# Performance work log

Hardware: AMD Instinct MI355X
Metric: run time of the kernel (lower is better)

The kernel has to match this reference:

```python
import math
import jax, jax.numpy as jnp
import numpy as np

N, C_S, C_Z, C, H, PQK, PV = 768, 384, 128, 16, 12, 4, 8
INF, EPS = 100000.0, 1e-8


def _quat_to_rot(q):
    # q: [N,4] normalized quaternions -> [N,3,3] rotation matrices
    w, x, y, z = q[:, 0], q[:, 1], q[:, 2], q[:, 3]
    return jnp.stack([
        jnp.stack([1 - 2 * (y * y + z * z), 2 * (x * y - w * z), 2 * (x * z + w * y)], -1),
        jnp.stack([2 * (x * y + w * z), 1 - 2 * (x * x + z * z), 2 * (y * z - w * x)], -1),
        jnp.stack([2 * (x * z - w * y), 2 * (y * z + w * x), 1 - 2 * (x * x + y * y)], -1),
    ], -2)


def setup_inputs() -> dict:
    key = jax.random.key(0)
    ks = jax.random.split(key, 16)
    quat = jax.random.normal(ks[2], (N, 4))
    quat = quat / jnp.linalg.norm(quat, axis=-1, keepdims=True)
    sc = 0.02
    return {
        "s": jax.random.normal(ks[0], (N, C_S), jnp.float32),
        "z": jax.random.normal(ks[1], (N, N, C_Z), jnp.float32),
        "rot": _quat_to_rot(quat).astype(jnp.float32),
        "trans": jax.random.normal(ks[3], (N, 3), jnp.float32),
        "mask": jnp.ones((N,), jnp.float32),
        "Wq": sc * jax.random.normal(ks[4], (C_S, H * C), jnp.float32),
        "bq": jnp.zeros((H * C,), jnp.float32),
        "Wqp": sc * jax.random.normal(ks[5], (C_S, H * 3 * PQK), jnp.float32),
        "bqp": jnp.zeros((H * 3 * PQK,), jnp.float32),
        "Wkv": sc * jax.random.normal(ks[6], (C_S, 2 * H * C), jnp.float32),
        "bkv": jnp.zeros((2 * H * C,), jnp.float32),
        "Wkvp": sc * jax.random.normal(ks[7], (C_S, H * 3 * (PQK + PV)), jnp.float32),
        "bkvp": jnp.zeros((H * 3 * (PQK + PV),), jnp.float32),
        "Wb": sc * jax.random.normal(ks[8], (C_Z, H), jnp.float32),
        "bb": jnp.zeros((H,), jnp.float32),
        "head_weights": 0.5413 * jnp.ones((H,), jnp.float32),  # softplus^{-1}(1)
        "Wout": sc * jax.random.normal(ks[9], (H * (C_Z + C + PV * 4), C_S), jnp.float32),
        "bout": jnp.zeros((C_S,), jnp.float32),
    }


def _proj_points(x, W, b, rot, trans, P):
    # PointProjection: split last dim into 3 coord chunks, stack as last axis
    pl = x @ W + b                                   # [N, H*3*P]
    pl = pl.reshape(-1, 3, H * P).transpose(0, 2, 1).reshape(-1, H, P, 3)
    return jnp.einsum('nij,nhpj->nhpi', rot, pl) + trans[:, None, None, :]


def reference(s, z, rot, trans, mask, Wq, bq, Wqp, bqp, Wkv, bkv, Wkvp, bkvp,
              Wb, bb, head_weights, Wout, bout):
    q = (s @ Wq + bq).reshape(N, H, C)
    kv = (s @ Wkv + bkv).reshape(N, H, 2 * C)
    k, v = kv[..., :C], kv[..., C:]
    q_pts = _proj_points(s, Wqp, bqp, rot, trans, PQK)          # [N,H,PQK,3]
    kv_pts = _proj_points(s, Wkvp, bkvp, rot, trans, PQK + PV)  # [N,H,PQK+PV,3]
    k_pts, v_pts = kv_pts[..., :PQK, :], kv_pts[..., PQK:, :]

    b_bias = z @ Wb + bb                                        # [N,N,H]
    a = jnp.einsum('qhc,khc->hqk', q, k) * math.sqrt(1.0 / (3 * C))
    a = a + math.sqrt(1.0 / 3) * jnp.transpose(b_bias, (2, 0, 1))

    # point-distance attention: [q,k,H,PQK]
    d2 = jnp.sum((q_pts[:, None] - k_pts[None]) ** 2, axis=-1)
    hw = jax.nn.softplus(head_weights) * math.sqrt(1.0 / (3 * (PQK * 9.0 / 2)))
    pt_att = -0.5 * jnp.sum(d2 * hw[:, None], axis=-1)          # [q,k,H]
    a = a + jnp.transpose(pt_att, (2, 0, 1))

    sq_mask = INF * (mask[:, None] * mask[None, :] - 1.0)       # [q,k]
    a = jax.nn.softmax(a + sq_mask[None], axis=-1)              # [H,q,k]

    o = jnp.einsum('hqk,khc->qhc', a, v).reshape(N, H * C)
    o_pt = jnp.einsum('hqk,khpd->qhpd', a, v_pts)               # [q,H,PV,3]
    o_pt = jnp.einsum('nji,nhpj->nhpi', rot, o_pt - trans[:, None, None, :])  # invert_apply
    o_pt_norm = jnp.sqrt(jnp.sum(o_pt ** 2, -1) + EPS).reshape(N, H * PV)
    o_pt_flat = o_pt.reshape(N, H * PV, 3)
    o_pair = jnp.einsum('hqk,qkc->qhc', a, z).reshape(N, H * C_Z)

    cat = jnp.concatenate(
        [o, o_pt_flat[..., 0], o_pt_flat[..., 1], o_pt_flat[..., 2], o_pt_norm, o_pair], -1)
    return cat @ Wout + bout
```

## Files before the change

kernel.cpp:

```cpp
#include <hip/hip_runtime.h>
#include <math.h>

#define NN    768
#define CS    384
#define INF_  100000.0f

#define OFF_Q       0
#define OFF_K       147456
#define OFF_V       294912
#define OFF_QPRAW   442368
#define OFF_KVPRAW  552960
#define OFF_QPTS    884736
#define OFF_KPTS    995328
#define OFF_VPTS    1105920
#define OFF_CAT     8414208

__global__ void __launch_bounds__(256)
k1_proj(const float* __restrict__ s,
        const float* __restrict__ Wq,  const float* __restrict__ bq,
        const float* __restrict__ Wqp, const float* __restrict__ bqp,
        const float* __restrict__ Wkv, const float* __restrict__ bkv,
        const float* __restrict__ Wkvp,const float* __restrict__ bkvp,
        float* __restrict__ ws) {
  __shared__ float s_lds[8][CS];
  const int n0 = blockIdx.y * 8;
  const int j0 = blockIdx.x * 32;
  const int t  = threadIdx.x;

  const float4* s4  = (const float4*)(s + (size_t)n0 * CS);
  float4*       sl4 = (float4*)(&s_lds[0][0]);
  for (int i = t; i < 768; i += 256) sl4[i] = s4[i];
  __syncthreads();

  const int m = t >> 5;
  const int j = j0 + (t & 31);

  const float* W; const float* bv; int jj, ncols;
  if (j < 192)      { W = Wq;   bv = bq;   jj = j;       ncols = 192; }
  else if (j < 576) { W = Wkv;  bv = bkv;  jj = j - 192; ncols = 384; }
  else if (j < 720) { W = Wqp;  bv = bqp;  jj = j - 576; ncols = 144; }
  else              { W = Wkvp; bv = bkvp; jj = j - 720; ncols = 432; }

  float acc = bv[jj];
  const float* Wp = W + jj;
  for (int c = 0; c < CS; ++c) acc += s_lds[m][c] * Wp[(size_t)c * ncols];

  const int n = n0 + m;
  if (j < 192) {
    (ws + OFF_Q)[n * 192 + jj] = acc;
  } else if (j < 576) {
    int h = jj >> 5, c = jj & 31;
    if (c < 16) (ws + OFF_K)[n * 192 + h * 16 + c] = acc;
    else        (ws + OFF_V)[n * 192 + h * 16 + (c - 16)] = acc;
  } else if (j < 720) {
    (ws + OFF_QPRAW)[n * 144 + jj] = acc;
  } else {
    (ws + OFF_KVPRAW)[n * 432 + jj] = acc;
  }
}

__global__ void __launch_bounds__(256)
k2_rot(const float* __restrict__ rot, const float* __restrict__ trans,
       float* __restrict__ ws) {
  const int idx = blockIdx.x * 256 + threadIdx.x;
  const int n = idx / 192;
  const int r = idx % 192;
  const float* R = rot + n * 9;
  const float* T = trans + n * 3;
  if (r < 48) {
    const float* raw = ws + OFF_QPRAW + n * 144;
    float p0 = raw[r], p1 = raw[48 + r], p2 = raw[96 + r];
    float g0 = R[0]*p0 + R[1]*p1 + R[2]*p2 + T[0];
    float g1 = R[3]*p0 + R[4]*p1 + R[5]*p2 + T[1];
    float g2 = R[6]*p0 + R[7]*p1 + R[8]*p2 + T[2];
    float* qp = ws + OFF_QPTS + n * 144 + r * 3;
    qp[0] = g0; qp[1] = g1; qp[2] = g2;
  } else {
    const int r2 = r - 48;
    const float* raw = ws + OFF_KVPRAW + n * 432;
    float p0 = raw[r2], p1 = raw[144 + r2], p2 = raw[288 + r2];
    float g0 = R[0]*p0 + R[1]*p1 + R[2]*p2 + T[0];
    float g1 = R[3]*p0 + R[4]*p1 + R[5]*p2 + T[1];
    float g2 = R[6]*p0 + R[7]*p1 + R[8]*p2 + T[2];
    const int h = r2 / 12, p = r2 % 12;
    if (p < 4) {
      float* kp = ws + OFF_KPTS + n * 144 + (h * 4 + p) * 3;
      kp[0] = g0; kp[1] = g1; kp[2] = g2;
    } else {
      float* vp = ws + OFF_VPTS + n * 288 + (h * 8 + (p - 4)) * 3;
      vp[0] = g0; vp[1] = g1; vp[2] = g2;
    }
  }
}

__global__ void __launch_bounds__(256, 4)
k3_fused(const float* __restrict__ z, const float* __restrict__ rot,
         const float* __restrict__ trans, const float* __restrict__ mask,
         const float* __restrict__ Wb, const float* __restrict__ bb,
         const float* __restrict__ hwin, float* __restrict__ ws) {
  const int q = blockIdx.x, t = threadIdx.x;
  const int g  = __builtin_amdgcn_readfirstlane(t >> 6);
  const int kl = t & 63;
  const int kx = kl & 31;

  __shared__ float4 z4[64][32];
  __shared__ float  w_s[64][12];
  __shared__ float  hw_l[12], bb_l[12], lsum[12], linv[12];
  __shared__ float  opt_raw[288];

  if (t < 12) {
    hw_l[t] = logf(1.0f + expf(hwin[t])) * 0.13608276348795434f;
    bb_l[t] = bb[t];
  }

  const float maskq  = mask[q];
  const float* qrow  = ws + OFF_Q    + q * 192;
  const float* qprow = ws + OFF_QPTS + q * 144;
  const float* kbase = ws + OFF_K;
  const float* kpbase= ws + OFF_KPTS;
  const float* vbase = ws + OFF_V;
  const float* vpbase= ws + OFF_VPTS;
  const float4* zg4  = (const float4*)z + (size_t)q * 24576;

  float l3[3] = {0.f, 0.f, 0.f};
  float op[12];
  #pragma unroll
  for (int j = 0; j < 12; ++j) op[j] = 0.f;
  float oa[4] = {0.f, 0.f, 0.f, 0.f};

  const int tt = t - 128;
  int o_c = 0, o_hq = 0, p_r = 0, p_hq = 0;
  if (tt >= 0 && tt < 48)        { o_c = tt & 15; o_hq = tt >> 4; }
  else if (tt >= 48 && tt < 120) { int jt = tt - 48; p_r = jt % 24; p_hq = jt / 24; }

  for (int k0 = 0; k0 < NN; k0 += 64) {
    __syncthreads();

    #pragma unroll
    for (int j = 0; j < 8; ++j) {
      const int i = t + 256 * j;
      const int row = i >> 5, c4 = i & 31;
      z4[row][c4 ^ (row & 31)] = zg4[k0 * 32 + i];
    }
    __syncthreads();

    {
      float b0 = 0.f, b1 = 0.f, b2 = 0.f;
      #pragma unroll 8
      for (int c4 = 0; c4 < 32; ++c4) {
        const float4 zv = z4[kl][c4 ^ kx];
        const float* wb = Wb + c4 * 48;
        b0 += zv.x*wb[g]    + zv.y*wb[12+g]  + zv.z*wb[24+g]  + zv.w*wb[36+g];
        b1 += zv.x*wb[4+g]  + zv.y*wb[16+g]  + zv.z*wb[28+g]  + zv.w*wb[40+g];
        b2 += zv.x*wb[8+g]  + zv.y*wb[20+g]  + zv.z*wb[32+g]  + zv.w*wb[44+g];
      }
      const int kg = k0 + kl;
      const float mterm = INF_ * (maskq * mask[kg] - 1.0f);
      const float* Kr  = kbase  + kg * 192;
      const float* KPr = kpbase + kg * 144;
      const float bias3[3] = {b0, b1, b2};
      #pragma unroll
      for (int j = 0; j < 3; ++j) {
        const int h = g + 4 * j;
        const float4* K4 = (const float4*)(Kr + h * 16);
        float qk = 0.f;
        #pragma unroll
        for (int c4i = 0; c4i < 4; ++c4i) {
          const float4 kv = K4[c4i];
          const float* qp = qrow + h * 16 + c4i * 4;
          qk += kv.x*qp[0] + kv.y*qp[1] + kv.z*qp[2] + kv.w*qp[3];
        }
        const float4* KP4 = (const float4*)(KPr + h * 12);
        float pt = 0.f;
        #pragma unroll
        for (int r = 0; r < 3; ++r) {
          const float4 kp = KP4[r];
          const float* qpp = qprow + h * 12 + r * 4;
          const float d0 = qpp[0]-kp.x, d1 = qpp[1]-kp.y, d2 = qpp[2]-kp.z, d3 = qpp[3]-kp.w;
          pt += d0*d0 + d1*d1 + d2*d2 + d3*d3;
        }
        const float logit = 0.14433756729740643f * qk
                          + 0.57735026918962576f * (bias3[j] + bb_l[h])
                          - 0.5f * hw_l[h] * pt + mterm;
        const float wv = __expf(logit);
        w_s[kl][h] = wv;
        l3[j] += wv;
      }
    }
    __syncthreads();

    if (t < 128) {
      float wreg[12];
      {
        const float4* wrow = (const float4*)&w_s[kl][0];
        const float4 wa = wrow[0], wbb = wrow[1], wc = wrow[2];
        wreg[0]=wa.x;  wreg[1]=wa.y;  wreg[2]=wa.z;  wreg[3]=wa.w;
        wreg[4]=wbb.x; wreg[5]=wbb.y; wreg[6]=wbb.z; wreg[7]=wbb.w;
        wreg[8]=wc.x;  wreg[9]=wc.y;  wreg[10]=wc.z; wreg[11]=wc.w;
      }
      const int cq = t >> 2, ce = t & 3;
      const float* zb = (const float*)z4;
      #pragma unroll 8
      for (int k = 0; k < 64; ++k) {
        const float zv = zb[k * 128 + ((cq ^ (k & 31)) << 2) + ce];
        #pragma unroll
        for (int j = 0; j < 12; ++j) {
          const float wkj = __uint_as_float(
              __builtin_amdgcn_readlane(__float_as_uint(wreg[j]), k));
          op[j] += wkj * zv;
        }
      }
    } else if (tt < 48) {
      const float* Vp = vbase + (o_hq * 4) * 16 + o_c;
      #pragma unroll 4
      for (int k = 0; k < 64; ++k) {
        const float4 wv4 = *(const float4*)&w_s[k][o_hq * 4];
        const float* vr = Vp + (size_t)(k0 + k) * 192;
        oa[0] += wv4.x * vr[0];
        oa[1] += wv4.y * vr[16];
        oa[2] += wv4.z * vr[32];
        oa[3] += wv4.w * vr[48];
      }
    } else if (tt < 120) {
      const float* VPp = vpbase + (p_hq * 4) * 24 + p_r;
      #pragma unroll 4
      for (int k = 0; k < 64; ++k) {
        const float4 wv4 = *(const float4*)&w_s[k][p_hq * 4];
        const float* vr = VPp + (size_t)(k0 + k) * 288;
        oa[0] += wv4.x * vr[0];
        oa[1] += wv4.y * vr[24];
        oa[2] += wv4.z * vr[48];
        oa[3] += wv4.w * vr[72];
      }
    }
  }

  #pragma unroll
  for (int j = 0; j < 3; ++j) {
    float v = l3[j];
    for (int off = 1; off < 64; off <<= 1) v += __shfl_xor(v, off, 64);
    l3[j] = v;
  }
  if ((t & 63) == 0) { lsum[g] = l3[0]; lsum[g + 4] = l3[1]; lsum[g + 8] = l3[2]; }
  __syncthreads();
  if (t < 12) linv[t] = 1.0f / lsum[t];
  __syncthreads();

  float* cat = ws + OFF_CAT + (size_t)q * 2112;
  if (t < 128) {
    #pragma unroll
    for (int j = 0; j < 12; ++j) cat[576 + j * 128 + t] = op[j] * linv[j];
  } else if (tt < 48) {
    #pragma unroll
    for (int e = 0; e < 4; ++e)
      cat[(o_hq * 4 + e) * 16 + o_c] = oa[e] * linv[o_hq * 4 + e];
  } else if (tt < 120) {
    #pragma unroll
    for (int e = 0; e < 4; ++e)
      opt_raw[(p_hq * 4 + e) * 24 + p_r] = oa[e] * linv[p_hq * 4 + e];
  }
  __syncthreads();

  if (t < 96) {
    const int h = t >> 3, p = t & 7;
    const float* R = rot + q * 9;
    const float* T = trans + q * 3;
    const float g0 = opt_raw[h * 24 + p * 3 + 0] - T[0];
    const float g1 = opt_raw[h * 24 + p * 3 + 1] - T[1];
    const float g2 = opt_raw[h * 24 + p * 3 + 2] - T[2];
    const float x  = R[0]*g0 + R[3]*g1 + R[6]*g2;
    const float y  = R[1]*g0 + R[4]*g1 + R[7]*g2;
    const float zc = R[2]*g0 + R[5]*g1 + R[8]*g2;
    const int hp = h * 8 + p;
    cat[192 + hp] = x;
    cat[288 + hp] = y;
    cat[384 + hp] = zc;
    cat[480 + hp] = sqrtf(x*x + y*y + zc*zc + 1e-8f);
  }
}

__global__ void __launch_bounds__(256)
k5_out(const float* __restrict__ Wout, const float* __restrict__ bout,
       const float* __restrict__ ws, float* __restrict__ out) {
  __shared__ float cat_lds[4 * 2112];
  const int m0 = blockIdx.y * 4;
  const int n0 = blockIdx.x * 64;
  const int t  = threadIdx.x;

  const float4* c4  = (const float4*)(ws + OFF_CAT + (size_t)m0 * 2112);
  float4*       cl4 = (float4*)cat_lds;
  for (int i = t; i < 2112; i += 256) cl4[i] = c4[i];
  __syncthreads();

  const int m = t >> 6, nn = n0 + (t & 63);
  const float* cm = cat_lds + m * 2112;
  float acc = bout[nn];
  for (int k = 0; k < 2112; ++k) acc += cm[k] * Wout[(size_t)k * 384 + nn];
  out[(size_t)(m0 + m) * 384 + nn] = acc;
}

extern "C" void kernel_launch(void* const* d_in, const int* in_sizes, int n_in,
                              void* d_out, int out_size, void* d_ws, size_t ws_size,
                              hipStream_t stream) {
  const float* s     = (const float*)d_in[0];
  const float* z     = (const float*)d_in[1];
  const float* rot   = (const float*)d_in[2];
  const float* trans = (const float*)d_in[3];
  const float* mask  = (const float*)d_in[4];
  const float* Wq    = (const float*)d_in[5];
  const float* bq    = (const float*)d_in[6];
  const float* Wqp   = (const float*)d_in[7];
  const float* bqp   = (const float*)d_in[8];
  const float* Wkv   = (const float*)d_in[9];
  const float* bkv   = (const float*)d_in[10];
  const float* Wkvp  = (const float*)d_in[11];
  const float* bkvp  = (const float*)d_in[12];
  const float* Wb    = (const float*)d_in[13];
  const float* bb    = (const float*)d_in[14];
  const float* hw    = (const float*)d_in[15];
  const float* Wout  = (const float*)d_in[16];
  const float* bout  = (const float*)d_in[17];
  float* out = (float*)d_out;
  float* ws  = (float*)d_ws;

  k1_proj<<<dim3(36, 96), 256, 0, stream>>>(s, Wq, bq, Wqp, bqp, Wkv, bkv, Wkvp, bkvp, ws);
  k2_rot <<<576, 256, 0, stream>>>(rot, trans, ws);
  k3_fused<<<NN, 256, 0, stream>>>(z, rot, trans, mask, Wb, bb, hw, ws);
  k5_out<<<dim3(6, 192), 256, 0, stream>>>(Wout, bout, ws, out);
}
```

Before: 797.5 us.

## Use bf16 MFMA for pair bias and pair output, tile output GEMM with split-K

The fused attention kernel now converts each z tile to bf16 in two LDS layouts and uses MFMA 16x16x32 instructions for both the z·Wb pair bias and the weighted sum over z. K and key points are pre-transposed by a new kernel so logits read coalesced columns. The work of accumulating over V and V-points is redistributed across all threads. The output projection becomes a 64x64 register-tiled GEMM with 4-way split-K and atomicAdd onto a bias-initialised output. bf16 rounding of z and of the attention weights lowers precision, and the atomics make the output order-dependent.

```diff
diff --git a/kernel.cpp b/kernel.cpp
--- a/kernel.cpp
+++ b/kernel.cpp
@@ -4,6 +4,9 @@
 #define NN    768
 #define CS    384
 #define INF_  100000.0f
+
+typedef __attribute__((ext_vector_type(8))) short s16x8;
+typedef __attribute__((ext_vector_type(4))) float f32x4;
 
 #define OFF_Q       0
 #define OFF_K       147456
@@ -13,7 +16,17 @@
 #define OFF_QPTS    884736
 #define OFF_KPTS    995328
 #define OFF_VPTS    1105920
+#define OFF_KT      1327104
+#define OFF_KPT     1474560
 #define OFF_CAT     8414208
+
+__device__ __forceinline__ unsigned short f2bf(float x) {
+  unsigned u = __float_as_uint(x) + 0x8000u;
+  return (unsigned short)(u >> 16);
+}
+__device__ __forceinline__ unsigned pk2(float a, float b) {
+  return (unsigned)f2bf(a) | ((unsigned)f2bf(b) << 16);
+}
 
 __global__ void __launch_bounds__(256)
 k1_proj(const float* __restrict__ s,
@@ -93,144 +106,174 @@
   }
 }
 
-__global__ void __launch_bounds__(256, 4)
+__global__ void __launch_bounds__(256)
+k2b_tr(float* __restrict__ ws) {
+  const int i = blockIdx.x * 256 + threadIdx.x;
+  if (i < 147456) {
+    const int n = i / 192, cc = i % 192;
+    (ws + OFF_KT)[cc * 768 + n] = (ws + OFF_K)[i];
+  } else {
+    const int i2 = i - 147456;
+    const int n = i2 / 144, r = i2 % 144;
+    (ws + OFF_KPT)[r * 768 + n] = (ws + OFF_KPTS)[i2];
+  }
+}
+
+#define ZT_S 72
+#define ZR_S 136
+#define WT_S 72
+#define WH_S 68
+__global__ void __launch_bounds__(256, 3)
 k3_fused(const float* __restrict__ z, const float* __restrict__ rot,
          const float* __restrict__ trans, const float* __restrict__ mask,
          const float* __restrict__ Wb, const float* __restrict__ bb,
          const float* __restrict__ hwin, float* __restrict__ ws) {
   const int q = blockIdx.x, t = threadIdx.x;
-  const int g  = __builtin_amdgcn_readfirstlane(t >> 6);
-  const int kl = t & 63;
-  const int kx = kl & 31;
-
-  __shared__ float4 z4[64][32];
-  __shared__ float  w_s[64][12];
-  __shared__ float  hw_l[12], bb_l[12], lsum[12], linv[12];
-  __shared__ float  opt_raw[288];
+  const int g   = t >> 6;
+  const int kl  = t & 63;
+  const int l15 = kl & 15, lq = kl >> 4;
+
+  __shared__ unsigned short zT[128 * ZT_S];
+  __shared__ unsigned short zR[64 * ZR_S];
+  __shared__ unsigned short wT[16 * WT_S];
+  __shared__ float wH[12 * WH_S];
+  __shared__ float bias_s[64 * 13];
+  __shared__ float hw_l[12], bb_l[12], lsum[12], linv[12];
+  __shared__ float opt_raw[288];
 
   if (t < 12) {
     hw_l[t] = logf(1.0f + expf(hwin[t])) * 0.13608276348795434f;
     bb_l[t] = bb[t];
   }
 
+  s16x8 wbA[4];
+  #pragma unroll
+  for (int kk = 0; kk < 4; ++kk) {
+    #pragma unroll
+    for (int j = 0; j < 8; ++j) {
+      float v = (l15 < 12) ? Wb[(kk * 32 + lq * 8 + j) * 12 + l15] : 0.0f;
+      wbA[kk][j] = (short)f2bf(v);
+    }
+  }
+
   const float maskq  = mask[q];
   const float* qrow  = ws + OFF_Q    + q * 192;
   const float* qprow = ws + OFF_QPTS + q * 144;
-  const float* kbase = ws + OFF_K;
-  const float* kpbase= ws + OFF_KPTS;
+  const float* ktr   = ws + OFF_KT;
+  const float* kptr  = ws + OFF_KPT;
   const float* vbase = ws + OFF_V;
   const float* vpbase= ws + OFF_VPTS;
   const float4* zg4  = (const float4*)z + (size_t)q * 24576;
 
   float l3[3] = {0.f, 0.f, 0.f};
-  float op[12];
-  #pragma unroll
-  for (int j = 0; j < 12; ++j) op[j] = 0.f;
-  float oa[4] = {0.f, 0.f, 0.f, 0.f};
-
-  const int tt = t - 128;
-  int o_c = 0, o_hq = 0, p_r = 0, p_hq = 0;
-  if (tt >= 0 && tt < 48)        { o_c = tt & 15; o_hq = tt >> 4; }
-  else if (tt >= 48 && tt < 120) { int jt = tt - 48; p_r = jt % 24; p_hq = jt / 24; }
+  f32x4 opA = {0.f,0.f,0.f,0.f}, opB = {0.f,0.f,0.f,0.f};
+  float o_acc = 0.f;
+  float pt0 = 0.f, pt1 = 0.f;
+  const int oh  = t >> 4;
+  const int ph  = t / 24,        prr = t % 24;
+  const int p2s = 256 + t, p2h = p2s / 24;
 
   for (int k0 = 0; k0 < NN; k0 += 64) {
     __syncthreads();
 
+    float4 zv[8];
+    #pragma unroll
+    for (int j = 0; j < 8; ++j) zv[j] = zg4[k0 * 32 + t + 256 * j];
+    const int kb = t >> 5, c4 = t & 31;
     #pragma unroll
     for (int j = 0; j < 8; ++j) {
-      const int i = t + 256 * j;
-      const int row = i >> 5, c4 = i & 31;
-      z4[row][c4 ^ (row & 31)] = zg4[k0 * 32 + i];
+      uint2 d;
+      d.x = pk2(zv[j].x, zv[j].y);
+      d.y = pk2(zv[j].z, zv[j].w);
+      *(uint2*)&zR[(kb + 8 * j) * ZR_S + c4 * 4] = d;
+    }
+    #pragma unroll
+    for (int e = 0; e < 4; ++e) {
+      uint4 d;
+      d.x = pk2(((const float*)&zv[0])[e], ((const float*)&zv[1])[e]);
+      d.y = pk2(((const float*)&zv[2])[e], ((const float*)&zv[3])[e]);
+      d.z = pk2(((const float*)&zv[4])[e], ((const float*)&zv[5])[e]);
+      d.w = pk2(((const float*)&zv[6])[e], ((const float*)&zv[7])[e]);
+      *(uint4*)&zT[(c4 * 4 + e) * ZT_S + kb * 8] = d;
     }
     __syncthreads();
 
     {
-      float b0 = 0.f, b1 = 0.f, b2 = 0.f;
-      #pragma unroll 8
-      for (int c4 = 0; c4 < 32; ++c4) {
-        const float4 zv = z4[kl][c4 ^ kx];
-        const float* wb = Wb + c4 * 48;
-        b0 += zv.x*wb[g]    + zv.y*wb[12+g]  + zv.z*wb[24+g]  + zv.w*wb[36+g];
-        b1 += zv.x*wb[4+g]  + zv.y*wb[16+g]  + zv.z*wb[28+g]  + zv.w*wb[40+g];
-        b2 += zv.x*wb[8+g]  + zv.y*wb[20+g]  + zv.z*wb[32+g]  + zv.w*wb[44+g];
+      f32x4 bd = {0.f,0.f,0.f,0.f};
+      #pragma unroll
+      for (int kk = 0; kk < 4; ++kk) {
+        s16x8 bf = *(const s16x8*)&zR[(g * 16 + l15) * ZR_S + kk * 32 + lq * 8];
+        bd = __builtin_amdgcn_mfma_f32_16x16x32_bf16(wbA[kk], bf, bd, 0, 0, 0);
       }
+      #pragma unroll
+      for (int r = 0; r < 4; ++r) {
+        const int h = lq * 4 + r;
+        if (h < 12) bias_s[(g * 16 + l15) * 13 + h] = bd[r];
+      }
+    }
+    float lg[3];
+    {
       const int kg = k0 + kl;
       const float mterm = INF_ * (maskq * mask[kg] - 1.0f);
-      const float* Kr  = kbase  + kg * 192;
-      const float* KPr = kpbase + kg * 144;
-      const float bias3[3] = {b0, b1, b2};
       #pragma unroll
       for (int j = 0; j < 3; ++j) {
         const int h = g + 4 * j;
-        const float4* K4 = (const float4*)(Kr + h * 16);
         float qk = 0.f;
         #pragma unroll
-        for (int c4i = 0; c4i < 4; ++c4i) {
-          const float4 kv = K4[c4i];
-          const float* qp = qrow + h * 16 + c4i * 4;
-          qk += kv.x*qp[0] + kv.y*qp[1] + kv.z*qp[2] + kv.w*qp[3];
-        }
-        const float4* KP4 = (const float4*)(KPr + h * 12);
+        for (int c = 0; c < 16; ++c)
+          qk += qrow[h * 16 + c] * ktr[(h * 16 + c) * 768 + kg];
         float pt = 0.f;
         #pragma unroll
-        for (int r = 0; r < 3; ++r) {
-          const float4 kp = KP4[r];
-          const float* qpp = qprow + h * 12 + r * 4;
-          const float d0 = qpp[0]-kp.x, d1 = qpp[1]-kp.y, d2 = qpp[2]-kp.z, d3 = qpp[3]-kp.w;
-          pt += d0*d0 + d1*d1 + d2*d2 + d3*d3;
+        for (int r = 0; r < 12; ++r) {
+          const float d = qprow[h * 12 + r] - kptr[(h * 12 + r) * 768 + kg];
+          pt += d * d;
         }
-        const float logit = 0.14433756729740643f * qk
-                          + 0.57735026918962576f * (bias3[j] + bb_l[h])
-                          - 0.5f * hw_l[h] * pt + mterm;
-        const float wv = __expf(logit);
-        w_s[kl][h] = wv;
-        l3[j] += wv;
+        lg[j] = 0.14433756729740643f * qk
+              + 0.57735026918962576f * bb_l[h]
+              - 0.5f * hw_l[h] * pt + mterm;
       }
     }
     __syncthreads();
 
-    if (t < 128) {
-      float wreg[12];
-      {
-        const float4* wrow = (const float4*)&w_s[kl][0];
-        const float4 wa = wrow[0], wbb = wrow[1], wc = wrow[2];
-        wreg[0]=wa.x;  wreg[1]=wa.y;  wreg[2]=wa.z;  wreg[3]=wa.w;
-        wreg[4]=wbb.x; wreg[5]=wbb.y; wreg[6]=wbb.z; wreg[7]=wbb.w;
-        wreg[8]=wc.x;  wreg[9]=wc.y;  wreg[10]=wc.z; wreg[11]=wc.w;
-      }
-      const int cq = t >> 2, ce = t & 3;
-      const float* zb = (const float*)z4;
-      #pragma unroll 8
-      for (int k = 0; k < 64; ++k) {
-        const float zv = zb[k * 128 + ((cq ^ (k & 31)) << 2) + ce];
-        #pragma unroll
-        for (int j = 0; j < 12; ++j) {
-          const float wkj = __uint_as_float(
-              __builtin_amdgcn_readlane(__float_as_uint(wreg[j]), k));
-          op[j] += wkj * zv;
+    #pragma unroll
+    for (int j = 0; j < 3; ++j) {
+      const int h = g + 4 * j;
+      const float wv = __expf(lg[j] + 0.57735026918962576f * bias_s[kl * 13 + h]);
+      l3[j] += wv;
+      wH[h * WH_S + kl] = wv;
+      wT[h * WT_S + (((kl & 7) << 3) | (kl >> 3))] = f2bf(wv);
+    }
+    __syncthreads();
+
+    #pragma unroll
+    for (int kk = 0; kk < 2; ++kk) {
+      s16x8 af = *(const s16x8*)&wT[l15 * WT_S + kk * 32 + lq * 8];
+      s16x8 b0 = *(const s16x8*)&zT[((2 * g)     * 16 + l15) * ZT_S + kk * 32 + lq * 8];
+      opA = __builtin_amdgcn_mfma_f32_16x16x32_bf16(af, b0, opA, 0, 0, 0);
+      s16x8 b1 = *(const s16x8*)&zT[((2 * g + 1) * 16 + l15) * ZT_S + kk * 32 + lq * 8];
+      opB = __builtin_amdgcn_mfma_f32_16x16x32_bf16(af, b1, opB, 0, 0, 0);
+    }
+    {
+      const float* vpr = vpbase + (size_t)k0 * 288;
+      const float* vr  = vbase  + (size_t)k0 * 192;
+      #pragma unroll 4
+      for (int k4 = 0; k4 < 16; ++k4) {
+        const int k = k4 * 4;
+        {
+          const float4 w4 = *(const float4*)&wH[ph * WH_S + k];
+          pt0 += w4.x * vpr[(k    ) * 288 + t] + w4.y * vpr[(k + 1) * 288 + t]
+               + w4.z * vpr[(k + 2) * 288 + t] + w4.w * vpr[(k + 3) * 288 + t];
         }
-      }
-    } else if (tt < 48) {
-      const float* Vp = vbase + (o_hq * 4) * 16 + o_c;
-      #pragma unroll 4
-      for (int k = 0; k < 64; ++k) {
-        const float4 wv4 = *(const float4*)&w_s[k][o_hq * 4];
-        const float* vr = Vp + (size_t)(k0 + k) * 192;
-        oa[0] += wv4.x * vr[0];
-        oa[1] += wv4.y * vr[16];
-        oa[2] += wv4.z * vr[32];
-        oa[3] += wv4.w * vr[48];
-      }
-    } else if (tt < 120) {
-      const float* VPp = vpbase + (p_hq * 4) * 24 + p_r;
-      #pragma unroll 4
-      for (int k = 0; k < 64; ++k) {
-        const float4 wv4 = *(const float4*)&w_s[k][p_hq * 4];
-        const float* vr = VPp + (size_t)(k0 + k) * 288;
-        oa[0] += wv4.x * vr[0];
-        oa[1] += wv4.y * vr[24];
-        oa[2] += wv4.z * vr[48];
-        oa[3] += wv4.w * vr[72];
+        if (t < 32) {
+          const float4 w4 = *(const float4*)&wH[p2h * WH_S + k];
+          pt1 += w4.x * vpr[(k    ) * 288 + p2s] + w4.y * vpr[(k + 1) * 288 + p2s]
+               + w4.z * vpr[(k + 2) * 288 + p2s] + w4.w * vpr[(k + 3) * 288 + p2s];
+        }
+        if (t < 192) {
+          const float4 w4 = *(const float4*)&wH[oh * WH_S + k];
+          o_acc += w4.x * vr[(k    ) * 192 + t] + w4.y * vr[(k + 1) * 192 + t]
+                 + w4.z * vr[(k + 2) * 192 + t] + w4.w * vr[(k + 3) * 192 + t];
+        }
       }
     }
   }
@@ -241,24 +284,23 @@
     for (int off = 1; off < 64; off <<= 1) v += __shfl_xor(v, off, 64);
     l3[j] = v;
   }
-  if ((t & 63) == 0) { lsum[g] = l3[0]; lsum[g + 4] = l3[1]; lsum[g + 8] = l3[2]; }
+  if (kl == 0) { lsum[g] = l3[0]; lsum[g + 4] = l3[1]; lsum[g + 8] = l3[2]; }
   __syncthreads();
   if (t < 12) linv[t] = 1.0f / lsum[t];
   __syncthreads();
 
   float* cat = ws + OFF_CAT + (size_t)q * 2112;
-  if (t < 128) {
-    #pragma unroll
-    for (int j = 0; j < 12; ++j) cat[576 + j * 128 + t] = op[j] * linv[j];
-  } else if (tt < 48) {
-    #pragma unroll
-    for (int e = 0; e < 4; ++e)
-      cat[(o_hq * 4 + e) * 16 + o_c] = oa[e] * linv[o_hq * 4 + e];
-  } else if (tt < 120) {
-    #pragma unroll
-    for (int e = 0; e < 4; ++e)
-      opt_raw[(p_hq * 4 + e) * 24 + p_r] = oa[e] * linv[p_hq * 4 + e];
-  }
+  #pragma unroll
+  for (int r = 0; r < 4; ++r) {
+    const int h = lq * 4 + r;
+    if (h < 12) {
+      cat[576 + h * 128 + (2 * g)     * 16 + l15] = opA[r] * linv[h];
+      cat[576 + h * 128 + (2 * g + 1) * 16 + l15] = opB[r] * linv[h];
+    }
+  }
+  if (t < 192) cat[t] = o_acc * linv[oh];
+  opt_raw[t] = pt0 * linv[ph];
+  if (t < 32) opt_raw[p2s] = pt1 * linv[p2h];
   __syncthreads();
 
   if (t < 96) {
@@ -280,23 +322,55 @@
 }
 
 __global__ void __launch_bounds__(256)
-k5_out(const float* __restrict__ Wout, const float* __restrict__ bout,
-       const float* __restrict__ ws, float* __restrict__ out) {
-  __shared__ float cat_lds[4 * 2112];
-  const int m0 = blockIdx.y * 4;
-  const int n0 = blockIdx.x * 64;
-  const int t  = threadIdx.x;
-
-  const float4* c4  = (const float4*)(ws + OFF_CAT + (size_t)m0 * 2112);
-  float4*       cl4 = (float4*)cat_lds;
-  for (int i = t; i < 2112; i += 256) cl4[i] = c4[i];
-  __syncthreads();
-
-  const int m = t >> 6, nn = n0 + (t & 63);
-  const float* cm = cat_lds + m * 2112;
-  float acc = bout[nn];
-  for (int k = 0; k < 2112; ++k) acc += cm[k] * Wout[(size_t)k * 384 + nn];
-  out[(size_t)(m0 + m) * 384 + nn] = acc;
+k5_init(const float* __restrict__ bout, float* __restrict__ out) {
+  const int i = blockIdx.x * 256 + threadIdx.x;
+  out[i] = bout[i % 384];
+}
+
+#define K5_CH 48
+__global__ void __launch_bounds__(256)
+k5_out(const float* __restrict__ Wout, const float* __restrict__ ws,
+       float* __restrict__ out) {
+  __shared__ float At[K5_CH * 68];
+  __shared__ float Bn[K5_CH * 68];
+  const int n0  = blockIdx.x * 64;
+  const int m0  = blockIdx.y * 64;
+  const int ks0 = blockIdx.z * 528;
+  const int t = threadIdx.x;
+  const int tx = t & 15, ty = t >> 4;
+  float acc[4][4] = {{0.f}};
+
+  const float* catg = ws + OFF_CAT;
+  for (int kc = 0; kc < 528; kc += K5_CH) {
+    __syncthreads();
+    #pragma unroll
+    for (int ii = 0; ii < 12; ++ii) {
+      const int i = t + 256 * ii;
+      const int m = i / 48, k = i % 48;
+      At[k * 68 + m] = catg[(size_t)(m0 + m) * 2112 + ks0 + kc + k];
+    }
+    #pragma unroll
+    for (int ii = 0; ii < 12; ++ii) {
+      const int i = t + 256 * ii;
+      const int k = i >> 6, n = i & 63;
+      Bn[k * 68 + n] = Wout[(size_t)(ks0 + kc + k) * 384 + n0 + n];
+    }
+    __syncthreads();
+    #pragma unroll 4
+    for (int k = 0; k < K5_CH; ++k) {
+      const float4 a4 = *(const float4*)&At[k * 68 + ty * 4];
+      const float4 b4 = *(const float4*)&Bn[k * 68 + tx * 4];
+      acc[0][0] += a4.x * b4.x; acc[0][1] += a4.x * b4.y; acc[0][2] += a4.x * b4.z; acc[0][3] += a4.x * b4.w;
+      acc[1][0] += a4.y * b4.x; acc[1][1] += a4.y * b4.y; acc[1][2] += a4.y * b4.z; acc[1][3] += a4.y * b4.w;
+      acc[2][0] += a4.z * b4.x; acc[2][1] += a4.z * b4.y; acc[2][2] += a4.z * b4.z; acc[2][3] += a4.z * b4.w;
+      acc[3][0] += a4.w * b4.x; acc[3][1] += a4.w * b4.y; acc[3][2] += a4.w * b4.z; acc[3][3] += a4.w * b4.w;
+    }
+  }
+  #pragma unroll
+  for (int r = 0; r < 4; ++r)
+    #pragma unroll
+    for (int c = 0; c < 4; ++c)
+      atomicAdd(&out[(size_t)(m0 + ty * 4 + r) * 384 + n0 + tx * 4 + c], acc[r][c]);
 }
 
 extern "C" void kernel_launch(void* const* d_in, const int* in_sizes, int n_in,
@@ -313,7 +387,7 @@
   const float* bqp   = (const float*)d_in[8];
   const float* Wkv   = (const float*)d_in[9];
   const float* bkv   = (const float*)d_in[10];
-  const float* Wkvp  = (const float*)d_in[11];
+  const float* bkvp_w= (const float*)d_in[11];
   const float* bkvp  = (const float*)d_in[12];
   const float* Wb    = (const float*)d_in[13];
   const float* bb    = (const float*)d_in[14];
@@ -323,8 +397,10 @@
   float* out = (float*)d_out;
   float* ws  = (float*)d_ws;
 
-  k1_proj<<<dim3(36, 96), 256, 0, stream>>>(s, Wq, bq, Wqp, bqp, Wkv, bkv, Wkvp, bkvp, ws);
+  k1_proj<<<dim3(36, 96), 256, 0, stream>>>(s, Wq, bq, Wqp, bqp, Wkv, bkv, bkvp_w, bkvp, ws);
   k2_rot <<<576, 256, 0, stream>>>(rot, trans, ws);
+  k2b_tr <<<1008, 256, 0, stream>>>(ws);
   k3_fused<<<NN, 256, 0, stream>>>(z, rot, trans, mask, Wb, bb, hw, ws);
-  k5_out<<<dim3(6, 192), 256, 0, stream>>>(Wout, bout, ws, out);
-}
+  k5_init<<<1152, 256, 0, stream>>>(bout, out);
+  k5_out<<<dim3(6, 12, 4), 256, 0, stream>>>(Wout, ws, out);
+}
```

New measurement: 837.8 us. 1.05x slower.
